# Optimization experiments

Measured on AMD Instinct MI355X. Metric: run time of the kernel, lower is better.

The kernel has to match this reference:

```python
import jax, jax.numpy as jnp
import numpy as np

SIGMA_INIT = 1000.0


def setup_inputs() -> dict:
    key = jax.random.key(0)
    k1, k2, k3 = jax.random.split(key, 3)
    B, M, D, S = 1024, 209, 12288, 2
    input_data = jax.random.normal(k1, (B, D), dtype=jnp.float32)
    center = jax.random.normal(k2, (M, D), dtype=jnp.float32)
    sigma = SIGMA_INIT * jnp.ones((M,), dtype=jnp.float32)
    W = 50.0 * jax.random.normal(k3, (S, M), dtype=jnp.float32)
    b = jnp.zeros((S,), dtype=jnp.float32)
    return {"input_data": input_data, "center": center, "sigma": sigma, "W": W, "b": b}


def reference(input_data, center, sigma, W, b):
    # Euclidean distance ||x_i - c_j|| via GEMM expansion (avoids [B,M,D] diff tensor)
    x2 = jnp.sum(input_data * input_data, axis=1, keepdims=True)        # [B,1]
    c2 = jnp.sum(center * center, axis=1)[None, :]                      # [1,M]
    d2 = x2 + c2 - 2.0 * (input_data @ center.T)                        # [B,M]
    dist = jnp.sqrt(jnp.maximum(d2, 0.0))
    # Note: original divides the (non-squared) norm by sigma^2, then exp(-.)
    radial = jnp.exp(-dist / (sigma * sigma)[None, :])                  # [B,M]
    return radial @ W.T + b                                             # [B,S]
```

## Files before the change

### kernel.cpp

```cpp
#include <hip/hip_runtime.h>
#include <hip/hip_bf16.h>
#include <stdint.h>

#define B_SZ 1024
#define M_SZ 209
#define MPAD 224
#define D_SZ 12288
#define KC   16
#define KCH  768
#define BK   128
#define NIT  (KCH / BK)
#define NB   32
#define BT   32
#define NCT  7
#define SROW 224
#define SLROW (KC * SROW)

#define CBF_OFF  0u
#define XXP_OFF  (MPAD * D_SZ)
#define CCP_OFF  (XXP_OFF + B_SZ * KC * 4)
#define SLAB_OFF (CCP_OFF + MPAD * 2 * 4)

typedef __attribute__((ext_vector_type(8))) short short8;
typedef __attribute__((ext_vector_type(4))) float floatx4;

__device__ __forceinline__ uint32_t pk8x4(const float4& v) {
    int d = __builtin_amdgcn_cvt_pk_fp8_f32(v.x, v.y, 0, false);
    d     = __builtin_amdgcn_cvt_pk_fp8_f32(v.z, v.w, d, true);
    return (uint32_t)d;
}

__device__ __forceinline__ void gload_lds16(const void* g, void* l) {
    __builtin_amdgcn_global_load_lds(
        (const __attribute__((address_space(1))) void*)g,
        (__attribute__((address_space(3))) void*)l, 16, 0, 0);
}

__global__ __launch_bounds__(256) void rbf_prep(
    const float* __restrict__ c, uint8_t* __restrict__ cf8,
    float* __restrict__ ccp)
{
    __shared__ float red[4];
    const int j = blockIdx.x >> 1, h = blockIdx.x & 1;
    const int t = threadIdx.x;
    const int base = h * (D_SZ / 2);
    uint8_t* dst = cf8 + (size_t)j * D_SZ + base;
    float s = 0.f;
    if (j < M_SZ) {
        const float* src = c + (size_t)j * D_SZ + base;
        for (int i = t * 8; i < D_SZ / 2; i += 2048) {
            float4 v0 = *(const float4*)(src + i);
            float4 v1 = *(const float4*)(src + i + 4);
            s += v0.x*v0.x + v0.y*v0.y + v0.z*v0.z + v0.w*v0.w
               + v1.x*v1.x + v1.y*v1.y + v1.z*v1.z + v1.w*v1.w;
            uint2 w = { pk8x4(v0), pk8x4(v1) };
            *(uint2*)(dst + i) = w;
        }
    } else {
        uint2 zz = {0u, 0u};
        for (int i = t * 8; i < D_SZ / 2; i += 2048) *(uint2*)(dst + i) = zz;
    }
#pragma unroll
    for (int off = 32; off > 0; off >>= 1) s += __shfl_down(s, off);
    if ((t & 63) == 0) red[t >> 6] = s;
    __syncthreads();
    if (t == 0) ccp[j * 2 + h] = red[0] + red[1] + red[2] + red[3];
}

__global__ __launch_bounds__(256, 2) void rbf_main(
    const float* __restrict__ x, const uint8_t* __restrict__ cf8,
    uint8_t* __restrict__ slab, float* __restrict__ xxp)
{
    __shared__ uint8_t sx[2][BT * BK];
    __shared__ uint8_t sc[2][MPAD * BK];

    const int t    = threadIdx.x;
    const int k    = blockIdx.x;
    const int b    = blockIdx.y;
    const int wave = t >> 6, lane = t & 63;
    const int quad = lane >> 4, mrow = lane & 15;
    const int qh = quad >> 1, ql = quad & 1;
    const int s2 = (mrow >> 1) & 7;
    const int rt  = wave & 1;
    const int cth = wave >> 1;

    floatx4 acc[NCT];
    const floatx4 z4 = {0.f, 0.f, 0.f, 0.f};
#pragma unroll
    for (int i = 0; i < NCT; ++i) acc[i] = z4;

    const int oE = (((lane & 7) ^ (lane >> 4)) & 7) * 16;
    const int oO = ((((lane & 7) ^ (lane >> 4)) ^ 4) & 7) * 16;
    const uint8_t* cpbE = cf8 + (size_t)(lane >> 3) * D_SZ + (size_t)k * KCH + oE;
    const uint8_t* cpbO = cf8 + (size_t)(lane >> 3) * D_SZ + (size_t)k * KCH + oO;

#pragma unroll
    for (int jj = 0; jj < 7; ++jj) {
        const int cr = wave * 7 + jj;
        const uint8_t* p = ((cr & 1) ? cpbO : cpbE) + (size_t)cr * 8 * D_SZ;
        gload_lds16(p, &sc[0][cr * 1024]);
    }

    const int xr = t >> 3;
    const int xc = t & 7;
    const float* xp = x + (size_t)(b * BT + xr) * D_SZ + (size_t)k * KCH + xc * 16;

    float4 ra0 = *(const float4*)(xp + 0);
    float4 ra1 = *(const float4*)(xp + 4);
    float4 ra2 = *(const float4*)(xp + 8);
    float4 ra3 = *(const float4*)(xp + 12);
    float4 rb0 = *(const float4*)(xp + BK + 0);
    float4 rb1 = *(const float4*)(xp + BK + 4);
    float4 rb2 = *(const float4*)(xp + BK + 8);
    float4 rb3 = *(const float4*)(xp + BK + 12);

    float sxx = ra0.x*ra0.x + ra0.y*ra0.y + ra0.z*ra0.z + ra0.w*ra0.w
              + ra1.x*ra1.x + ra1.y*ra1.y + ra1.z*ra1.z + ra1.w*ra1.w
              + ra2.x*ra2.x + ra2.y*ra2.y + ra2.z*ra2.z + ra2.w*ra2.w
              + ra3.x*ra3.x + ra3.y*ra3.y + ra3.z*ra3.z + ra3.w*ra3.w;

    const int sxoff = xr * BK + ((xc ^ ((xr >> 1) & 7)) & 7) * 16;
    {
        uint4 xw0 = make_uint4(pk8x4(ra0), pk8x4(ra1), pk8x4(ra2), pk8x4(ra3));
        *(uint4*)&sx[0][sxoff] = xw0;
    }

    int boff[4];
#pragma unroll
    for (int ks = 0; ks < 4; ++ks)
        boff[ks] = (((ks * 2 + qh) ^ s2) & 7) * 16 + ql * 8;
    const int aoff  = (rt * 16 + mrow) * BK;
    const int boff0 = (cth * 7 * 16 + mrow) * BK;

    __syncthreads();

#pragma unroll
    for (int it = 0; it < NIT; ++it) {
        const int cur = it & 1;
        if (it + 1 < NIT) {
            sxx += rb0.x*rb0.x + rb0.y*rb0.y + rb0.z*rb0.z + rb0.w*rb0.w
                 + rb1.x*rb1.x + rb1.y*rb1.y + rb1.z*rb1.z + rb1.w*rb1.w
                 + rb2.x*rb2.x + rb2.y*rb2.y + rb2.z*rb2.z + rb2.w*rb2.w
                 + rb3.x*rb3.x + rb3.y*rb3.y + rb3.z*rb3.z + rb3.w*rb3.w;
            uint4 xwn = make_uint4(pk8x4(rb0), pk8x4(rb1), pk8x4(rb2), pk8x4(rb3));
            *(uint4*)&sx[cur ^ 1][sxoff] = xwn;
            if (it + 2 < NIT) {
                const float* q = xp + (it + 2) * BK;
                rb0 = *(const float4*)(q + 0);
                rb1 = *(const float4*)(q + 4);
                rb2 = *(const float4*)(q + 8);
                rb3 = *(const float4*)(q + 12);
            }
#pragma unroll
            for (int jj = 0; jj < 7; ++jj) {
                const int cr = wave * 7 + jj;
                const uint8_t* p = ((cr & 1) ? cpbO : cpbE)
                                 + (size_t)cr * 8 * D_SZ + (it + 1) * BK;
                gload_lds16(p, &sc[cur ^ 1][cr * 1024]);
            }
        }
#pragma unroll
        for (int ks = 0; ks < 4; ++ks) {
            const long a = *(const long*)(&sx[cur][aoff] + boff[ks]);
#pragma unroll
            for (int ct = 0; ct < NCT; ++ct) {
                const long bv = *(const long*)(&sc[cur][boff0] + ct * 16 * BK + boff[ks]);
                acc[ct] = __builtin_amdgcn_mfma_f32_16x16x32_fp8_fp8(a, bv, acc[ct], 0, 0, 0);
            }
        }
        __syncthreads();
    }

    {
        uint8_t* sd = slab + (size_t)k * SROW;
        const int gi0 = b * BT + rt * 16 + quad * 4;
#pragma unroll
        for (int ct = 0; ct < NCT; ++ct) {
            const int gj = (cth * 7 + ct) * 16 + mrow;
            const int p01 = __builtin_amdgcn_cvt_pk_fp8_f32(acc[ct][0], acc[ct][1], 0, false);
            const int p23 = __builtin_amdgcn_cvt_pk_fp8_f32(acc[ct][2], acc[ct][3], 0, false);
            uint8_t* wb = sd + (size_t)gi0 * SLROW + gj;
            wb[0]                 = (uint8_t)(p01 & 0xff);
            wb[SLROW]             = (uint8_t)((p01 >> 8) & 0xff);
            wb[2 * (size_t)SLROW] = (uint8_t)(p23 & 0xff);
            wb[3 * (size_t)SLROW] = (uint8_t)((p23 >> 8) & 0xff);
        }
        sxx += __shfl_down(sxx, 4);
        sxx += __shfl_down(sxx, 2);
        sxx += __shfl_down(sxx, 1);
        if ((t & 7) == 0) xxp[(size_t)(b * BT + xr) * KC + k] = sxx;
    }
}

__global__ __launch_bounds__(256) void rbf_fin(
    const uint8_t* __restrict__ slab, const float* __restrict__ xxp,
    const float* __restrict__ ccp, const float* __restrict__ sigma,
    const float* __restrict__ W, const float* __restrict__ bias,
    float* __restrict__ out)
{
    __shared__ float jpart[MPAD * 9];
    __shared__ float jtot[MPAD];
    __shared__ float xsh;

    const int t = threadIdx.x;
    const int i = blockIdx.x;

    if (t < 64) {
        float xv = (t < KC) ? xxp[(size_t)i * KC + t] : 0.f;
#pragma unroll
        for (int off = 32; off > 0; off >>= 1) xv += __shfl_down(xv, off);
        if (t == 0) xsh = xv;
    }

    const int o = t % 28, g = t / 28;
    if (t < 252) {
        const uint8_t* sp = slab + (size_t)i * SLROW + o * 8;
        float s8[8] = {0.f,0.f,0.f,0.f,0.f,0.f,0.f,0.f};
        for (int kk = g; kk < KC; kk += 9) {
            uint2 v = *(const uint2*)(sp + (size_t)kk * SROW);
            s8[0] += __builtin_amdgcn_cvt_f32_fp8((int)v.x, 0);
            s8[1] += __builtin_amdgcn_cvt_f32_fp8((int)v.x, 1);
            s8[2] += __builtin_amdgcn_cvt_f32_fp8((int)v.x, 2);
            s8[3] += __builtin_amdgcn_cvt_f32_fp8((int)v.x, 3);
            s8[4] += __builtin_amdgcn_cvt_f32_fp8((int)v.y, 0);
            s8[5] += __builtin_amdgcn_cvt_f32_fp8((int)v.y, 1);
            s8[6] += __builtin_amdgcn_cvt_f32_fp8((int)v.y, 2);
            s8[7] += __builtin_amdgcn_cvt_f32_fp8((int)v.y, 3);
        }
#pragma unroll
        for (int e = 0; e < 8; ++e) jpart[(o * 8 + e) * 9 + g] = s8[e];
    }
    __syncthreads();

    if (t < MPAD) {
        float d = 0.f;
#pragma unroll
        for (int g2 = 0; g2 < 9; ++g2) d += jpart[t * 9 + g2];
        jtot[t] = d;
    }
    __syncthreads();

    if (t < 64) {
        const float xxi = xsh;
        float a0 = 0.f, a1 = 0.f;
        for (int j = t; j < M_SZ; j += 64) {
            const float ccj = ccp[j * 2] + ccp[j * 2 + 1];
            float d2 = fmaxf(xxi + ccj - 2.f * jtot[j], 0.f);
            float sg = sigma[j];
            float rad = __expf(-sqrtf(d2) / (sg * sg));
            a0 += rad * W[j];
            a1 += rad * W[M_SZ + j];
        }
#pragma unroll
        for (int off = 32; off > 0; off >>= 1) {
            a0 += __shfl_down(a0, off);
            a1 += __shfl_down(a1, off);
        }
        if (t == 0) {
            out[i * 2 + 0] = a0 + bias[0];
            out[i * 2 + 1] = a1 + bias[1];
        }
    }
}

extern "C" void kernel_launch(void* const* d_in, const int* in_sizes, int n_in,
                              void* d_out, int out_size, void* d_ws, size_t ws_size,
                              hipStream_t stream)
{
    const float* x     = (const float*)d_in[0];
    const float* c     = (const float*)d_in[1];
    const float* sigma = (const float*)d_in[2];
    const float* W     = (const float*)d_in[3];
    const float* bias  = (const float*)d_in[4];
    float* out = (float*)d_out;

    char* ws = (char*)d_ws;
    uint8_t* cf8  = (uint8_t*)(ws + CBF_OFF);
    float*   xxp  = (float*)(ws + XXP_OFF);
    float*   ccp  = (float*)(ws + CCP_OFF);
    uint8_t* slab = (uint8_t*)(ws + SLAB_OFF);

    rbf_prep<<<MPAD * 2, 256, 0, stream>>>(c, cf8, ccp);
    rbf_main<<<dim3(KC, NB), 256, 0, stream>>>(x, cf8, slab, xxp);
    rbf_fin<<<B_SZ, 256, 0, stream>>>(slab, xxp, ccp, sigma, W, bias, out);
}
```

Before: 108.9 us.

## Halve K tile to 64 and raise occupancy to five blocks per CU

Shrinks the per-iteration K tile from 128 to 64 bytes, which halves LDS per block and the number of x registers held. This allows launch bounds of 5 blocks per CU instead of 2. The center-tile LDS load is remapped to 16-row chunks split 4/4/3/3 across waves, with an adjusted 4-way swizzle. It also adds sched barriers and skips the final syncthreads. The goal is better latency hiding through occupancy, at the cost of twice as many iterations and barriers per K chunk.

Result: slower. 141.7 us (+30.2%).

```diff
diff --git a/kernel.cpp b/kernel.cpp
--- a/kernel.cpp
+++ b/kernel.cpp
@@ -8,7 +8,7 @@
 #define D_SZ 12288
 #define KC   16
 #define KCH  768
-#define BK   128
+#define BK   64
 #define NIT  (KCH / BK)
 #define NB   32
 #define BT   32
@@ -67,7 +67,7 @@
     if (t == 0) ccp[j * 2 + h] = red[0] + red[1] + red[2] + red[3];
 }
 
-__global__ __launch_bounds__(256, 2) void rbf_main(
+__global__ __launch_bounds__(256, 5) void rbf_main(
     const float* __restrict__ x, const uint8_t* __restrict__ cf8,
     uint8_t* __restrict__ slab, float* __restrict__ xxp)
 {
@@ -80,7 +80,7 @@
     const int wave = t >> 6, lane = t & 63;
     const int quad = lane >> 4, mrow = lane & 15;
     const int qh = quad >> 1, ql = quad & 1;
-    const int s2 = (mrow >> 1) & 7;
+    const int s2 = (mrow >> 1) & 3;
     const int rt  = wave & 1;
     const int cth = wave >> 1;
 
@@ -89,46 +89,43 @@
 #pragma unroll
     for (int i = 0; i < NCT; ++i) acc[i] = z4;
 
-    const int oE = (((lane & 7) ^ (lane >> 4)) & 7) * 16;
-    const int oO = ((((lane & 7) ^ (lane >> 4)) ^ 4) & 7) * 16;
-    const uint8_t* cpbE = cf8 + (size_t)(lane >> 3) * D_SZ + (size_t)k * KCH + oE;
-    const uint8_t* cpbO = cf8 + (size_t)(lane >> 3) * D_SZ + (size_t)k * KCH + oO;
-
-#pragma unroll
-    for (int jj = 0; jj < 7; ++jj) {
-        const int cr = wave * 7 + jj;
-        const uint8_t* p = ((cr & 1) ? cpbO : cpbE) + (size_t)cr * 8 * D_SZ;
-        gload_lds16(p, &sc[0][cr * 1024]);
-    }
+    const int crs = (wave < 2) ? wave * 4 : 8 + (wave - 2) * 3;
+    const int crn = (wave < 2) ? 4 : 3;
+    const uint8_t* cpb = cf8 + (size_t)(lane >> 2) * D_SZ + (size_t)k * KCH
+                       + (((lane & 3) ^ ((lane >> 3) & 3)) * 16);
+
+#pragma unroll
+    for (int jj = 0; jj < 4; ++jj) {
+        if (jj < crn) {
+            const int cr = crs + jj;
+            gload_lds16(cpb + (size_t)cr * 16 * D_SZ, &sc[0][cr * 1024]);
+        }
+    }
+    __builtin_amdgcn_sched_barrier(0);
 
     const int xr = t >> 3;
     const int xc = t & 7;
-    const float* xp = x + (size_t)(b * BT + xr) * D_SZ + (size_t)k * KCH + xc * 16;
+    const float* xp = x + (size_t)(b * BT + xr) * D_SZ + (size_t)k * KCH + xc * 8;
 
     float4 ra0 = *(const float4*)(xp + 0);
     float4 ra1 = *(const float4*)(xp + 4);
-    float4 ra2 = *(const float4*)(xp + 8);
-    float4 ra3 = *(const float4*)(xp + 12);
     float4 rb0 = *(const float4*)(xp + BK + 0);
     float4 rb1 = *(const float4*)(xp + BK + 4);
-    float4 rb2 = *(const float4*)(xp + BK + 8);
-    float4 rb3 = *(const float4*)(xp + BK + 12);
 
     float sxx = ra0.x*ra0.x + ra0.y*ra0.y + ra0.z*ra0.z + ra0.w*ra0.w
-              + ra1.x*ra1.x + ra1.y*ra1.y + ra1.z*ra1.z + ra1.w*ra1.w
-              + ra2.x*ra2.x + ra2.y*ra2.y + ra2.z*ra2.z + ra2.w*ra2.w
-              + ra3.x*ra3.x + ra3.y*ra3.y + ra3.z*ra3.z + ra3.w*ra3.w;
-
-    const int sxoff = xr * BK + ((xc ^ ((xr >> 1) & 7)) & 7) * 16;
+              + ra1.x*ra1.x + ra1.y*ra1.y + ra1.z*ra1.z + ra1.w*ra1.w;
+
+    const int sxoff = xr * BK + (((xc >> 1) ^ ((xr >> 1) & 3)) & 3) * 16
+                    + (xc & 1) * 8;
     {
-        uint4 xw0 = make_uint4(pk8x4(ra0), pk8x4(ra1), pk8x4(ra2), pk8x4(ra3));
-        *(uint4*)&sx[0][sxoff] = xw0;
-    }
-
-    int boff[4];
-#pragma unroll
-    for (int ks = 0; ks < 4; ++ks)
-        boff[ks] = (((ks * 2 + qh) ^ s2) & 7) * 16 + ql * 8;
+        uint2 xw0 = { pk8x4(ra0), pk8x4(ra1) };
+        *(uint2*)&sx[0][sxoff] = xw0;
+    }
+
+    int boff[2];
+#pragma unroll
+    for (int ks = 0; ks < 2; ++ks)
+        boff[ks] = (((ks * 2 + qh) ^ s2) & 3) * 16 + ql * 8;
     const int aoff  = (rt * 16 + mrow) * BK;
     const int boff0 = (cth * 7 * 16 + mrow) * BK;
 
@@ -139,28 +136,26 @@
         const int cur = it & 1;
         if (it + 1 < NIT) {
             sxx += rb0.x*rb0.x + rb0.y*rb0.y + rb0.z*rb0.z + rb0.w*rb0.w
-                 + rb1.x*rb1.x + rb1.y*rb1.y + rb1.z*rb1.z + rb1.w*rb1.w
-                 + rb2.x*rb2.x + rb2.y*rb2.y + rb2.z*rb2.z + rb2.w*rb2.w
-                 + rb3.x*rb3.x + rb3.y*rb3.y + rb3.z*rb3.z + rb3.w*rb3.w;
-            uint4 xwn = make_uint4(pk8x4(rb0), pk8x4(rb1), pk8x4(rb2), pk8x4(rb3));
-            *(uint4*)&sx[cur ^ 1][sxoff] = xwn;
+                 + rb1.x*rb1.x + rb1.y*rb1.y + rb1.z*rb1.z + rb1.w*rb1.w;
+            uint2 xwn = { pk8x4(rb0), pk8x4(rb1) };
+            *(uint2*)&sx[cur ^ 1][sxoff] = xwn;
+#pragma unroll
+            for (int jj = 0; jj < 4; ++jj) {
+                if (jj < crn) {
+                    const int cr = crs + jj;
+                    gload_lds16(cpb + (size_t)cr * 16 * D_SZ + (it + 1) * BK,
+                                &sc[cur ^ 1][cr * 1024]);
+                }
+            }
+            __builtin_amdgcn_sched_barrier(0);
             if (it + 2 < NIT) {
                 const float* q = xp + (it + 2) * BK;
                 rb0 = *(const float4*)(q + 0);
                 rb1 = *(const float4*)(q + 4);
-                rb2 = *(const float4*)(q + 8);
-                rb3 = *(const float4*)(q + 12);
             }
-#pragma unroll
-            for (int jj = 0; jj < 7; ++jj) {
-                const int cr = wave * 7 + jj;
-                const uint8_t* p = ((cr & 1) ? cpbO : cpbE)
-                                 + (size_t)cr * 8 * D_SZ + (it + 1) * BK;
-                gload_lds16(p, &sc[cur ^ 1][cr * 1024]);
-            }
-        }
-#pragma unroll
-        for (int ks = 0; ks < 4; ++ks) {
+        }
+#pragma unroll
+        for (int ks = 0; ks < 2; ++ks) {
             const long a = *(const long*)(&sx[cur][aoff] + boff[ks]);
 #pragma unroll
             for (int ct = 0; ct < NCT; ++ct) {
@@ -168,7 +163,7 @@
                 acc[ct] = __builtin_amdgcn_mfma_f32_16x16x32_fp8_fp8(a, bv, acc[ct], 0, 0, 0);
             }
         }
-        __syncthreads();
+        if (it + 1 < NIT) __syncthreads();
     }
 
     {
```
